# Performance work log

Measured on AMD Instinct MI355X. Metric: run time of the kernel, lower is better.

Reference implementation:

```python
import jax, jax.numpy as jnp
import numpy as np

N_NODES = 50000
N_EDGES = 800000
D = 128
NEG_SLOPE = 0.01
LN_EPS = 1e-5


def gcn_conv(x, W, b, src, dst, n_nodes):
    # Linear transform: [N, D_in] @ [D_in, D_out]
    h = x @ W
    # Symmetric degree normalization (self-loops already included in src/dst)
    deg = jax.ops.segment_sum(jnp.ones_like(dst, dtype=h.dtype), dst, num_segments=n_nodes)
    dinv = jnp.where(deg > 0, jax.lax.rsqrt(deg), 0.0)
    coef = dinv[src] * dinv[dst]                      # [E]
    msg = h[src] * coef[:, None]                      # gather + scale, [E, D]
    out = jax.ops.segment_sum(msg, dst, num_segments=n_nodes)  # scatter-add
    return out + b


def layer_norm(x, gamma, beta):
    mu = jnp.mean(x, axis=-1, keepdims=True)
    var = jnp.mean(jnp.square(x - mu), axis=-1, keepdims=True)
    return (x - mu) * jax.lax.rsqrt(var + LN_EPS) * gamma + beta


def setup_inputs() -> dict:
    key = jax.random.key(0)
    ks = jax.random.split(key, 8)
    x = jax.random.normal(ks[0], (N_NODES, D), dtype=jnp.float32)
    edge_index = jax.random.randint(ks[1], (2, N_EDGES), 0, N_NODES, dtype=jnp.int64)
    s = 1.0 / np.sqrt(D)
    W1 = jax.random.uniform(ks[2], (D, D), jnp.float32, -s, s)
    b1 = jnp.zeros((D,), jnp.float32)
    W2 = jax.random.uniform(ks[3], (D, D), jnp.float32, -s, s)
    b2 = jnp.zeros((D,), jnp.float32)
    ln1_g = jnp.ones((D,), jnp.float32)
    ln1_b = jnp.zeros((D,), jnp.float32)
    ln2_g = jnp.ones((D,), jnp.float32)
    ln2_b = jnp.zeros((D,), jnp.float32)
    return {"x": x, "edge_index": edge_index, "W1": W1, "b1": b1,
            "ln1_g": ln1_g, "ln1_b": ln1_b, "W2": W2, "b2": b2,
            "ln2_g": ln2_g, "ln2_b": ln2_b}


def reference(x, edge_index, W1, b1, ln1_g, ln1_b, W2, b2, ln2_g, ln2_b):
    n = x.shape[0]
    # add self-loops (PyG GCNConv default)
    loops = jnp.arange(n, dtype=edge_index.dtype)
    src = jnp.concatenate([edge_index[0], loops])
    dst = jnp.concatenate([edge_index[1], loops])

    residual = x
    h = gcn_conv(x, W1, b1, src, dst, n)
    h = jax.nn.leaky_relu(h, NEG_SLOPE)
    h = layer_norm(h + residual, ln1_g, ln1_b)
    h = gcn_conv(h, W2, b2, src, dst, n)
    return jax.nn.leaky_relu(layer_norm(h + residual, ln2_g, ln2_b), NEG_SLOPE)
```

## Files before the change

kernel.cpp:

```cpp
#include <hip/hip_runtime.h>
#include <hip/hip_bf16.h>

#define NN 50000
#define NE 800000
#define D 128
#define NEG_SLOPE 0.01f
#define LN_EPS 1e-5f

#define NPB 256
#define NB 196
#define CAP 6144
#define ECH 8192
#define NCH ((NE + ECH - 1) / ECH)

typedef __attribute__((ext_vector_type(8))) short bf16x8;
typedef __attribute__((ext_vector_type(4))) float f32x4;
typedef __attribute__((ext_vector_type(4))) int i32x4;

__device__ inline unsigned short f2bf(float f) {
    unsigned u = __float_as_uint(f);
    unsigned r = 0x7FFFu + ((u >> 16) & 1u);
    return (unsigned short)((u + r) >> 16);
}
__device__ inline void bf2x(unsigned u, float& lo, float& hi) {
    lo = __uint_as_float(u << 16);
    hi = __uint_as_float(u & 0xFFFF0000u);
}


__global__ __launch_bounds__(256) void bucket_scatter(const int* __restrict__ src,
                                                      const int* __restrict__ dst,
                                                      int* __restrict__ bcursor,
                                                      int2* __restrict__ bedge, int ne) {
    __shared__ int2 stage[ECH];
    __shared__ int hist[NB], lofs[NB], lcur[NB], gbase[NB];
    __shared__ int tmp[256];
    int t = threadIdx.x;
    int e0 = blockIdx.x * ECH;
    int ecnt = min(ECH, ne - e0);
    if (t < NB) hist[t] = 0;
    __syncthreads();
    for (int k = t; k < ecnt; k += 256) atomicAdd(&hist[dst[e0 + k] >> 8], 1);
    __syncthreads();
    int v = (t < NB) ? hist[t] : 0;
    tmp[t] = v;
    __syncthreads();
    for (int off = 1; off < 256; off <<= 1) {
        int u = (t >= off) ? tmp[t - off] : 0;
        __syncthreads();
        tmp[t] += u;
        __syncthreads();
    }
    if (t < NB) {
        lofs[t] = tmp[t] - v;
        lcur[t] = tmp[t] - v;
        gbase[t] = atomicAdd(&bcursor[t], v);
    }
    __syncthreads();
    for (int k = t; k < ecnt; k += 256) {
        int s = src[e0 + k], d = dst[e0 + k];
        int p = atomicAdd(&lcur[d >> 8], 1);
        stage[p] = make_int2(s, d);
    }
    __syncthreads();
    for (int k = t; k < ecnt; k += 256) {
        int2 eg = stage[k];
        int b = eg.y >> 8;
        bedge[(size_t)b * CAP + gbase[b] + (k - lofs[b])] = eg;
    }
}

__global__ __launch_bounds__(256) void node_count(const int2* __restrict__ bedge,
                                                  const int* __restrict__ bcnt,
                                                  float* __restrict__ dinv,
                                                  int2* __restrict__ rowinfo,
                                                  int* __restrict__ ticket) {
    __shared__ int h[NPB];
    __shared__ int tmp[256];
    __shared__ int base;
    int b = blockIdx.x, t = threadIdx.x;
    h[t] = 0;
    __syncthreads();
    int s0 = b * CAP, s1 = s0 + bcnt[b];
    for (int k = s0 + t; k < s1; k += 256) atomicAdd(&h[bedge[k].y & 255], 1);
    __syncthreads();
    int deg = h[t];
    int node = b * NPB + t;
    int pdeg = (deg + 7) & ~7;
    tmp[t] = pdeg;
    __syncthreads();
    for (int off = 1; off < 256; off <<= 1) {
        int u = (t >= off) ? tmp[t - off] : 0;
        __syncthreads();
        tmp[t] += u;
        __syncthreads();
    }
    if (t == 255) base = atomicAdd(ticket, tmp[255]);
    __syncthreads();
    if (node < NN) {
        dinv[node] = rsqrtf((float)(deg + 1));
        rowinfo[node] = make_int2(base + tmp[t] - pdeg, pdeg);
    }
}

__global__ __launch_bounds__(256) void csr_scatter(const int2* __restrict__ bedge,
                                                   const int* __restrict__ bcnt,
                                                   const int2* __restrict__ rowinfo,
                                                   const float* __restrict__ dinv,
                                                   int2* __restrict__ csr_pair) {
    __shared__ int cur[NPB];
    __shared__ int rl[NPB];
    int b = blockIdx.x, t = threadIdx.x;
    int node = b * NPB + t;
    rl[t] = (node < NN) ? rowinfo[node].x : 0;
    cur[t] = 0;
    __syncthreads();
    int s0 = b * CAP, s1 = s0 + bcnt[b];
    for (int k = s0 + t; k < s1; k += 256) {
        int2 eg = bedge[k];
        int li = eg.y & 255;
        int p = atomicAdd(&cur[li], 1);
        float coef = dinv[eg.x] * dinv[eg.y];
        csr_pair[rl[li] + p] = make_int2(eg.x, __float_as_int(coef));
    }
    __syncthreads();
    int deg = cur[t];
    int pend = (deg + 7) & ~7;
    int selfsrc = (node < NN) ? node : 0;
    for (int k = deg; k < pend; ++k)
        csr_pair[rl[t] + k] = make_int2(selfsrc, 0);
}

__global__ void wt_pack2(const float* __restrict__ W1, const float* __restrict__ W2,
                         unsigned short* __restrict__ WT1, unsigned short* __restrict__ WT2) {
    int tid = blockIdx.x * 256 + threadIdx.x;
    const float* W = (tid < D * D) ? W1 : W2;
    unsigned short* WT = (tid < D * D) ? WT1 : WT2;
    int id = tid & (D * D - 1);
    int nn = id & 127, k = id >> 7;
    WT[nn * 128 + k] = f2bf(W[k * 128 + nn]);
}

template <bool BF16IN>
__global__ __launch_bounds__(256) void gemm_mfma(const void* __restrict__ Ain,
                                                 const unsigned short* __restrict__ WT,
                                                 unsigned short* __restrict__ out, int n) {
    __shared__ __align__(16) unsigned short a_lds[64 * 128];
    __shared__ __align__(16) unsigned short w_lds[128 * 128];
    int t = threadIdx.x;
    int m0 = blockIdx.x * 64;

    #pragma unroll
    for (int it = 0; it < 8; ++it) {
        int idx = it * 256 + t;
        int row = idx >> 4, c = idx & 15;
        uint4 v = *(const uint4*)&WT[row * 128 + c * 8];
        int byte = (row * 256 + c * 16) ^ ((row & 7) << 4);
        *(uint4*)((char*)w_lds + byte) = v;
    }
    #pragma unroll
    for (int it = 0; it < 4; ++it) {
        int idx = it * 256 + t;
        int row = idx >> 4, c = idx & 15;
        int grow = m0 + row;
        uint4 w = make_uint4(0u, 0u, 0u, 0u);
        if (grow < n) {
            if constexpr (BF16IN) {
                w = *(const uint4*)&((const unsigned short*)Ain)[(size_t)grow * D + c * 8];
            } else {
                const float* Af = (const float*)Ain;
                float4 v0 = *(const float4*)&Af[(size_t)grow * D + c * 8];
                float4 v1 = *(const float4*)&Af[(size_t)grow * D + c * 8 + 4];
                w.x = (unsigned)f2bf(v0.x) | ((unsigned)f2bf(v0.y) << 16);
                w.y = (unsigned)f2bf(v0.z) | ((unsigned)f2bf(v0.w) << 16);
                w.z = (unsigned)f2bf(v1.x) | ((unsigned)f2bf(v1.y) << 16);
                w.w = (unsigned)f2bf(v1.z) | ((unsigned)f2bf(v1.w) << 16);
            }
        }
        int byte = (row * 256 + c * 16) ^ ((row & 7) << 4);
        *(uint4*)((char*)a_lds + byte) = w;
    }
    __syncthreads();

    int wv = t >> 6, l = t & 63;
    int lrow = l & 15, lgrp = l >> 4;
    int arow = wv * 16 + lrow;

    f32x4 acc[8];
    #pragma unroll
    for (int nf = 0; nf < 8; ++nf) acc[nf] = (f32x4){0.f, 0.f, 0.f, 0.f};

    #pragma unroll
    for (int kk = 0; kk < 4; ++kk) {
        int abyte = (arow * 256 + kk * 64 + lgrp * 16) ^ ((arow & 7) << 4);
        bf16x8 afrag = *(bf16x8*)((char*)a_lds + abyte);
        #pragma unroll
        for (int nf = 0; nf < 8; ++nf) {
            int bcol = nf * 16 + lrow;
            int bbyte = (bcol * 256 + kk * 64 + lgrp * 16) ^ ((bcol & 7) << 4);
            bf16x8 bfrag = *(bf16x8*)((char*)w_lds + bbyte);
            acc[nf] = __builtin_amdgcn_mfma_f32_16x16x32_bf16(afrag, bfrag, acc[nf], 0, 0, 0);
        }
    }

    #pragma unroll
    for (int nf = 0; nf < 8; ++nf) {
        #pragma unroll
        for (int r = 0; r < 4; ++r) {
            int grow = m0 + wv * 16 + lgrp * 4 + r;
            if (grow < n) {
                int col = nf * 16 + lrow;
                out[(size_t)grow * D + col] = f2bf(acc[nf][r]);
            }
        }
    }
}


__device__ inline void agg8(const unsigned* __restrict__ h, const int2* __restrict__ csr_pair,
                            int e, int lane, float& accx, float& accy) {
    i32x4 q0 = __builtin_nontemporal_load((const i32x4*)(csr_pair + e + 0));
    i32x4 q1 = __builtin_nontemporal_load((const i32x4*)(csr_pair + e + 2));
    i32x4 q2 = __builtin_nontemporal_load((const i32x4*)(csr_pair + e + 4));
    i32x4 q3 = __builtin_nontemporal_load((const i32x4*)(csr_pair + e + 6));
    unsigned g0 = h[(size_t)q0[0] * (D / 2) + lane];
    unsigned g1 = h[(size_t)q0[2] * (D / 2) + lane];
    unsigned g2 = h[(size_t)q1[0] * (D / 2) + lane];
    unsigned g3 = h[(size_t)q1[2] * (D / 2) + lane];
    unsigned g4 = h[(size_t)q2[0] * (D / 2) + lane];
    unsigned g5 = h[(size_t)q2[2] * (D / 2) + lane];
    unsigned g6 = h[(size_t)q3[0] * (D / 2) + lane];
    unsigned g7 = h[(size_t)q3[2] * (D / 2) + lane];
    float ax, ay, c;
    c = __int_as_float(q0[1]); bf2x(g0, ax, ay); accx = fmaf(c, ax, accx); accy = fmaf(c, ay, accy);
    c = __int_as_float(q0[3]); bf2x(g1, ax, ay); accx = fmaf(c, ax, accx); accy = fmaf(c, ay, accy);
    c = __int_as_float(q1[1]); bf2x(g2, ax, ay); accx = fmaf(c, ax, accx); accy = fmaf(c, ay, accy);
    c = __int_as_float(q1[3]); bf2x(g3, ax, ay); accx = fmaf(c, ax, accx); accy = fmaf(c, ay, accy);
    c = __int_as_float(q2[1]); bf2x(g4, ax, ay); accx = fmaf(c, ax, accx); accy = fmaf(c, ay, accy);
    c = __int_as_float(q2[3]); bf2x(g5, ax, ay); accx = fmaf(c, ax, accx); accy = fmaf(c, ay, accy);
    c = __int_as_float(q3[1]); bf2x(g6, ax, ay); accx = fmaf(c, ax, accx); accy = fmaf(c, ay, accy);
    c = __int_as_float(q3[3]); bf2x(g7, ax, ay); accx = fmaf(c, ax, accx); accy = fmaf(c, ay, accy);
}

template <int MODE>
__global__ __launch_bounds__(256) void agg_ln(const unsigned* __restrict__ h,
                                              const float* __restrict__ x,
                                              const float* __restrict__ bias,
                                              const float* __restrict__ gamma,
                                              const float* __restrict__ beta,
                                              const float* __restrict__ dinv,
                                              const int2* __restrict__ rowinfo,
                                              const int2* __restrict__ csr_pair,
                                              float* __restrict__ out,
                                              unsigned* __restrict__ outb) {
    int wid = threadIdx.x >> 6;
    int lane = threadIdx.x & 63;
    int iA = blockIdx.x * 8 + wid * 2;
    int iB = iA + 1;
    float diA = dinv[iA], diB = dinv[iB];

    float hx, hy;
    bf2x(h[(size_t)iA * (D / 2) + lane], hx, hy);
    float aAx = diA * diA * hx, aAy = diA * diA * hy;
    bf2x(h[(size_t)iB * (D / 2) + lane], hx, hy);
    float aBx = diB * diB * hx, aBy = diB * diB * hy;

    int2 riA = rowinfo[iA];
    int2 riB = rowinfo[iB];
    int eA = __builtin_amdgcn_readfirstlane(riA.x);
    int eA1 = eA + __builtin_amdgcn_readfirstlane(riA.y);
    int eB = __builtin_amdgcn_readfirstlane(riB.x);
    int eB1 = eB + __builtin_amdgcn_readfirstlane(riB.y);

    while (eA < eA1 && eB < eB1) {
        i32x4 qA0 = __builtin_nontemporal_load((const i32x4*)(csr_pair + eA + 0));
        i32x4 qA1 = __builtin_nontemporal_load((const i32x4*)(csr_pair + eA + 2));
        i32x4 qA2 = __builtin_nontemporal_load((const i32x4*)(csr_pair + eA + 4));
        i32x4 qA3 = __builtin_nontemporal_load((const i32x4*)(csr_pair + eA + 6));
        i32x4 qB0 = __builtin_nontemporal_load((const i32x4*)(csr_pair + eB + 0));
        i32x4 qB1 = __builtin_nontemporal_load((const i32x4*)(csr_pair + eB + 2));
        i32x4 qB2 = __builtin_nontemporal_load((const i32x4*)(csr_pair + eB + 4));
        i32x4 qB3 = __builtin_nontemporal_load((const i32x4*)(csr_pair + eB + 6));
        unsigned gA0 = h[(size_t)qA0[0] * (D / 2) + lane];
        unsigned gA1 = h[(size_t)qA0[2] * (D / 2) + lane];
        unsigned gA2 = h[(size_t)qA1[0] * (D / 2) + lane];
        unsigned gA3 = h[(size_t)qA1[2] * (D / 2) + lane];
        unsigned gA4 = h[(size_t)qA2[0] * (D / 2) + lane];
        unsigned gA5 = h[(size_t)qA2[2] * (D / 2) + lane];
        unsigned gA6 = h[(size_t)qA3[0] * (D / 2) + lane];
        unsigned gA7 = h[(size_t)qA3[2] * (D / 2) + lane];
        unsigned gB0 = h[(size_t)qB0[0] * (D / 2) + lane];
        unsigned gB1 = h[(size_t)qB0[2] * (D / 2) + lane];
        unsigned gB2 = h[(size_t)qB1[0] * (D / 2) + lane];
        unsigned gB3 = h[(size_t)qB1[2] * (D / 2) + lane];
        unsigned gB4 = h[(size_t)qB2[0] * (D / 2) + lane];
        unsigned gB5 = h[(size_t)qB2[2] * (D / 2) + lane];
        unsigned gB6 = h[(size_t)qB3[0] * (D / 2) + lane];
        unsigned gB7 = h[(size_t)qB3[2] * (D / 2) + lane];
        float ax, ay, c;
        c = __int_as_float(qA0[1]); bf2x(gA0, ax, ay); aAx = fmaf(c, ax, aAx); aAy = fmaf(c, ay, aAy);
        c = __int_as_float(qA0[3]); bf2x(gA1, ax, ay); aAx = fmaf(c, ax, aAx); aAy = fmaf(c, ay, aAy);
        c = __int_as_float(qA1[1]); bf2x(gA2, ax, ay); aAx = fmaf(c, ax, aAx); aAy = fmaf(c, ay, aAy);
        c = __int_as_float(qA1[3]); bf2x(gA3, ax, ay); aAx = fmaf(c, ax, aAx); aAy = fmaf(c, ay, aAy);
        c = __int_as_float(qA2[1]); bf2x(gA4, ax, ay); aAx = fmaf(c, ax, aAx); aAy = fmaf(c, ay, aAy);
        c = __int_as_float(qA2[3]); bf2x(gA5, ax, ay); aAx = fmaf(c, ax, aAx); aAy = fmaf(c, ay, aAy);
        c = __int_as_float(qA3[1]); bf2x(gA6, ax, ay); aAx = fmaf(c, ax, aAx); aAy = fmaf(c, ay, aAy);
        c = __int_as_float(qA3[3]); bf2x(gA7, ax, ay); aAx = fmaf(c, ax, aAx); aAy = fmaf(c, ay, aAy);
        c = __int_as_float(qB0[1]); bf2x(gB0, ax, ay); aBx = fmaf(c, ax, aBx); aBy = fmaf(c, ay, aBy);
        c = __int_as_float(qB0[3]); bf2x(gB1, ax, ay); aBx = fmaf(c, ax, aBx); aBy = fmaf(c, ay, aBy);
        c = __int_as_float(qB1[1]); bf2x(gB2, ax, ay); aBx = fmaf(c, ax, aBx); aBy = fmaf(c, ay, aBy);
        c = __int_as_float(qB1[3]); bf2x(gB3, ax, ay); aBx = fmaf(c, ax, aBx); aBy = fmaf(c, ay, aBy);
        c = __int_as_float(qB2[1]); bf2x(gB4, ax, ay); aBx = fmaf(c, ax, aBx); aBy = fmaf(c, ay, aBy);
        c = __int_as_float(qB2[3]); bf2x(gB5, ax, ay); aBx = fmaf(c, ax, aBx); aBy = fmaf(c, ay, aBy);
        c = __int_as_float(qB3[1]); bf2x(gB6, ax, ay); aBx = fmaf(c, ax, aBx); aBy = fmaf(c, ay, aBy);
        c = __int_as_float(qB3[3]); bf2x(gB7, ax, ay); aBx = fmaf(c, ax, aBx); aBy = fmaf(c, ay, aBy);
        eA += 8; eB += 8;
    }
    while (eA < eA1) { agg8(h, csr_pair, eA, lane, aAx, aAy); eA += 8; }
    while (eB < eB1) { agg8(h, csr_pair, eB, lane, aBx, aBy); eB += 8; }

    float2 bv = *(const float2*)&bias[2 * lane];
    float2 gv = *(const float2*)&gamma[2 * lane];
    float2 bt = *(const float2*)&beta[2 * lane];

    aAx += bv.x; aAy += bv.y;
    aBx += bv.x; aBy += bv.y;
    if (MODE == 0) {
        aAx = aAx > 0.f ? aAx : NEG_SLOPE * aAx;
        aAy = aAy > 0.f ? aAy : NEG_SLOPE * aAy;
        aBx = aBx > 0.f ? aBx : NEG_SLOPE * aBx;
        aBy = aBy > 0.f ? aBy : NEG_SLOPE * aBy;
    }
    size_t rowA = (size_t)iA * D + 2 * lane;
    size_t rowB = (size_t)iB * D + 2 * lane;
    float2 xA = *(const float2*)&x[rowA];
    float2 xB = *(const float2*)&x[rowB];
    float vA0 = aAx + xA.x, vA1 = aAy + xA.y;
    float vB0 = aBx + xB.x, vB1 = aBy + xB.y;

    float sA1 = vA0 + vA1, sA2 = vA0 * vA0 + vA1 * vA1;
    float sB1 = vB0 + vB1, sB2 = vB0 * vB0 + vB1 * vB1;
    #pragma unroll
    for (int off = 1; off < 64; off <<= 1) {
        sA1 += __shfl_xor(sA1, off, 64);
        sA2 += __shfl_xor(sA2, off, 64);
        sB1 += __shfl_xor(sB1, off, 64);
        sB2 += __shfl_xor(sB2, off, 64);
    }
    float muA = sA1 * (1.f / 128.f);
    float varA = fmaxf(sA2 * (1.f / 128.f) - muA * muA, 0.f);
    float rsA = rsqrtf(varA + LN_EPS);
    float muB = sB1 * (1.f / 128.f);
    float varB = fmaxf(sB2 * (1.f / 128.f) - muB * muB, 0.f);
    float rsB = rsqrtf(varB + LN_EPS);

    float oA0 = (vA0 - muA) * rsA * gv.x + bt.x;
    float oA1 = (vA1 - muA) * rsA * gv.y + bt.y;
    float oB0 = (vB0 - muB) * rsB * gv.x + bt.x;
    float oB1 = (vB1 - muB) * rsB * gv.y + bt.y;

    if (MODE == 0) {
        outb[(size_t)iA * (D / 2) + lane] = (unsigned)f2bf(oA0) | ((unsigned)f2bf(oA1) << 16);
        outb[(size_t)iB * (D / 2) + lane] = (unsigned)f2bf(oB0) | ((unsigned)f2bf(oB1) << 16);
    } else {
        oA0 = oA0 > 0.f ? oA0 : NEG_SLOPE * oA0;
        oA1 = oA1 > 0.f ? oA1 : NEG_SLOPE * oA1;
        oB0 = oB0 > 0.f ? oB0 : NEG_SLOPE * oB0;
        oB1 = oB1 > 0.f ? oB1 : NEG_SLOPE * oB1;
        *(float2*)&out[rowA] = make_float2(oA0, oA1);
        *(float2*)&out[rowB] = make_float2(oB0, oB1);
    }
}

extern "C" void kernel_launch(void* const* d_in, const int* in_sizes, int n_in,
                              void* d_out, int out_size, void* d_ws, size_t ws_size,
                              hipStream_t stream) {
    const float* x    = (const float*)d_in[0];
    const int*   ei   = (const int*)d_in[1];
    const float* W1   = (const float*)d_in[2];
    const float* b1   = (const float*)d_in[3];
    const float* ln1g = (const float*)d_in[4];
    const float* ln1b = (const float*)d_in[5];
    const float* W2   = (const float*)d_in[6];
    const float* b2   = (const float*)d_in[7];
    const float* ln2g = (const float*)d_in[8];
    const float* ln2b = (const float*)d_in[9];
    float* out = (float*)d_out;

    const int* srcp = ei;
    const int* dstp = ei + NE;

    char* ws = (char*)d_ws;
    size_t p = 0;
    auto alloc = [&](size_t bytes) {
        char* r = ws + p;
        p += (bytes + 255) & ~(size_t)255;
        return r;
    };
    int*   bcursor  = (int*)alloc((NB + 1) * 4);
    int2*  rowinfo  = (int2*)alloc((size_t)NN * 8);
    float* dinv     = (float*)alloc(NN * 4);
    int2*  bedge    = (int2*)alloc((size_t)NB * CAP * 8);
    int2*  csr_pair = (int2*)alloc(((size_t)NE + 8 * NN) * 8);
    unsigned short* hbf  = (unsigned short*)alloc((size_t)NN * D * 2);
    unsigned*       t1bf = (unsigned*)alloc((size_t)NN * D * 2);
    unsigned short* wt1  = (unsigned short*)alloc(D * D * 2);
    unsigned short* wt2  = (unsigned short*)alloc(D * D * 2);

    hipMemsetAsync(bcursor, 0, (NB + 1) * 4, stream);

    bucket_scatter<<<NCH, 256, 0, stream>>>(srcp, dstp, bcursor, bedge, NE);
    node_count<<<NB, 256, 0, stream>>>(bedge, bcursor, dinv, rowinfo, &bcursor[NB]);
    csr_scatter<<<NB, 256, 0, stream>>>(bedge, bcursor, rowinfo, dinv, csr_pair);

    wt_pack2<<<2 * D * D / 256, 256, 0, stream>>>(W1, W2, wt1, wt2);

    gemm_mfma<false><<<(NN + 63) / 64, 256, 0, stream>>>(x, wt1, hbf, NN);
    agg_ln<0><<<NN / 8, 256, 0, stream>>>((const unsigned*)hbf, x, b1, ln1g, ln1b, dinv,
                                          rowinfo, csr_pair, out, t1bf);

    gemm_mfma<true><<<(NN + 63) / 64, 256, 0, stream>>>(t1bf, wt2, hbf, NN);
    agg_ln<1><<<NN / 8, 256, 0, stream>>>((const unsigned*)hbf, x, b2, ln2g, ln2b, dinv,
                                          rowinfo, csr_pair, out, t1bf);
}
```

Measured before the change: 148.1 us.

## Fuse graph build with first GEMM and second GEMM into layer-1 aggregation

Edge bucketing, a global-atomic degree count and the first GEMM now run as independent block ranges inside one launch. Node counting and CSR scatter are merged into one kernel that reads degrees directly. The second GEMM is fused into the layer-1 aggregation/LayerNorm kernel, using 512-thread blocks that stage 16 normalized rows in LDS and run MFMA against W2 held in LDS. This cuts the launch count and removes the round trip of the intermediate bf16 activation through global memory. The cost is global atomics on degrees and reloading the 32KB W2 tile in every 16-row block.

```diff
diff --git a/kernel.cpp b/kernel.cpp
--- a/kernel.cpp
+++ b/kernel.cpp
@@ -10,8 +10,10 @@
 #define NPB 256
 #define NB 196
 #define CAP 6144
-#define ECH 8192
+#define ECH 6144
 #define NCH ((NE + ECH - 1) / ECH)
+#define NDEG 256
+#define NGEMM ((NN + 63) / 64)
 
 typedef __attribute__((ext_vector_type(8))) short bf16x8;
 typedef __attribute__((ext_vector_type(4))) float f32x4;
@@ -28,106 +30,180 @@
 }
 
 
-__global__ __launch_bounds__(256) void bucket_scatter(const int* __restrict__ src,
-                                                      const int* __restrict__ dst,
-                                                      int* __restrict__ bcursor,
-                                                      int2* __restrict__ bedge, int ne) {
-    __shared__ int2 stage[ECH];
-    __shared__ int hist[NB], lofs[NB], lcur[NB], gbase[NB];
+struct BucketLDS {
+    int2 stage[ECH];
+    int hist[NB], lofs[NB], lcur[NB], gbase[NB];
+    int tmp[256];
+};
+struct GemmLDS {
+    unsigned short a[64 * 128];
+    unsigned short w[128 * 128];
+};
+union FusedLDS { BucketLDS b; GemmLDS g; };
+
+__device__ inline void gemm_body(GemmLDS& L, const float* __restrict__ A,
+                                 const unsigned short* __restrict__ WT,
+                                 unsigned short* __restrict__ out, int m0, int n, int t) {
+    #pragma unroll
+    for (int it = 0; it < 8; ++it) {
+        int idx = it * 256 + t;
+        int row = idx >> 4, c = idx & 15;
+        uint4 v = *(const uint4*)&WT[row * 128 + c * 8];
+        int byte = (row * 256 + c * 16) ^ ((row & 7) << 4);
+        *(uint4*)((char*)L.w + byte) = v;
+    }
+    #pragma unroll
+    for (int it = 0; it < 4; ++it) {
+        int idx = it * 256 + t;
+        int row = idx >> 4, c = idx & 15;
+        int grow = m0 + row;
+        uint4 w = make_uint4(0u, 0u, 0u, 0u);
+        if (grow < n) {
+            float4 v0 = *(const float4*)&A[(size_t)grow * D + c * 8];
+            float4 v1 = *(const float4*)&A[(size_t)grow * D + c * 8 + 4];
+            w.x = (unsigned)f2bf(v0.x) | ((unsigned)f2bf(v0.y) << 16);
+            w.y = (unsigned)f2bf(v0.z) | ((unsigned)f2bf(v0.w) << 16);
+            w.z = (unsigned)f2bf(v1.x) | ((unsigned)f2bf(v1.y) << 16);
+            w.w = (unsigned)f2bf(v1.z) | ((unsigned)f2bf(v1.w) << 16);
+        }
+        int byte = (row * 256 + c * 16) ^ ((row & 7) << 4);
+        *(uint4*)((char*)L.a + byte) = w;
+    }
+    __syncthreads();
+
+    int wv = t >> 6, l = t & 63;
+    int lrow = l & 15, lgrp = l >> 4;
+    int arow = wv * 16 + lrow;
+
+    f32x4 acc[8];
+    #pragma unroll
+    for (int nf = 0; nf < 8; ++nf) acc[nf] = (f32x4){0.f, 0.f, 0.f, 0.f};
+
+    #pragma unroll
+    for (int kk = 0; kk < 4; ++kk) {
+        int abyte = (arow * 256 + kk * 64 + lgrp * 16) ^ ((arow & 7) << 4);
+        bf16x8 afrag = *(bf16x8*)((char*)L.a + abyte);
+        #pragma unroll
+        for (int nf = 0; nf < 8; ++nf) {
+            int bcol = nf * 16 + lrow;
+            int bbyte = (bcol * 256 + kk * 64 + lgrp * 16) ^ ((bcol & 7) << 4);
+            bf16x8 bfrag = *(bf16x8*)((char*)L.w + bbyte);
+            acc[nf] = __builtin_amdgcn_mfma_f32_16x16x32_bf16(afrag, bfrag, acc[nf], 0, 0, 0);
+        }
+    }
+
+    #pragma unroll
+    for (int nf = 0; nf < 8; ++nf) {
+        #pragma unroll
+        for (int r = 0; r < 4; ++r) {
+            int grow = m0 + wv * 16 + lgrp * 4 + r;
+            if (grow < n) out[(size_t)grow * D + nf * 16 + lrow] = f2bf(acc[nf][r]);
+        }
+    }
+}
+
+__global__ __launch_bounds__(256) void fused1(const int* __restrict__ src,
+                                              const int* __restrict__ dst,
+                                              int* __restrict__ bcursor,
+                                              int2* __restrict__ bedge,
+                                              int* __restrict__ deg,
+                                              const float* __restrict__ x,
+                                              const unsigned short* __restrict__ wt1,
+                                              unsigned short* __restrict__ hbf) {
+    __shared__ FusedLDS u;
+    int bid = blockIdx.x, t = threadIdx.x;
+
+    if (bid < NCH) {
+        BucketLDS& L = u.b;
+        int e0 = bid * ECH;
+        int ecnt = min(ECH, NE - e0);
+        if (t < NB) L.hist[t] = 0;
+        __syncthreads();
+        for (int k = t; k < ecnt; k += 256) atomicAdd(&L.hist[dst[e0 + k] >> 8], 1);
+        __syncthreads();
+        int v = (t < NB) ? L.hist[t] : 0;
+        L.tmp[t] = v;
+        __syncthreads();
+        for (int off = 1; off < 256; off <<= 1) {
+            int uu = (t >= off) ? L.tmp[t - off] : 0;
+            __syncthreads();
+            L.tmp[t] += uu;
+            __syncthreads();
+        }
+        if (t < NB) {
+            L.lofs[t] = L.tmp[t] - v;
+            L.lcur[t] = L.tmp[t] - v;
+            L.gbase[t] = atomicAdd(&bcursor[t], v);
+        }
+        __syncthreads();
+        for (int k = t; k < ecnt; k += 256) {
+            int s = src[e0 + k], d = dst[e0 + k];
+            int p = atomicAdd(&L.lcur[d >> 8], 1);
+            L.stage[p] = make_int2(s, d);
+        }
+        __syncthreads();
+        for (int k = t; k < ecnt; k += 256) {
+            int2 eg = L.stage[k];
+            int b = eg.y >> 8;
+            bedge[(size_t)b * CAP + L.gbase[b] + (k - L.lofs[b])] = eg;
+        }
+    } else if (bid < NCH + NDEG) {
+        for (int k = (bid - NCH) * 256 + t; k < NE; k += NDEG * 256)
+            atomicAdd(&deg[dst[k]], 1);
+    } else {
+        gemm_body(u.g, x, wt1, hbf, (bid - NCH - NDEG) * 64, NN, t);
+    }
+}
+
+__global__ __launch_bounds__(256) void fused2(const int2* __restrict__ bedge,
+                                              const int* __restrict__ bcnt,
+                                              const int* __restrict__ deg,
+                                              float* __restrict__ dinv,
+                                              int2* __restrict__ rowinfo,
+                                              int* __restrict__ ticket,
+                                              int2* __restrict__ csr_pair) {
     __shared__ int tmp[256];
-    int t = threadIdx.x;
-    int e0 = blockIdx.x * ECH;
-    int ecnt = min(ECH, ne - e0);
-    if (t < NB) hist[t] = 0;
-    __syncthreads();
-    for (int k = t; k < ecnt; k += 256) atomicAdd(&hist[dst[e0 + k] >> 8], 1);
-    __syncthreads();
-    int v = (t < NB) ? hist[t] : 0;
-    tmp[t] = v;
-    __syncthreads();
-    for (int off = 1; off < 256; off <<= 1) {
-        int u = (t >= off) ? tmp[t - off] : 0;
-        __syncthreads();
-        tmp[t] += u;
-        __syncthreads();
-    }
-    if (t < NB) {
-        lofs[t] = tmp[t] - v;
-        lcur[t] = tmp[t] - v;
-        gbase[t] = atomicAdd(&bcursor[t], v);
-    }
-    __syncthreads();
-    for (int k = t; k < ecnt; k += 256) {
-        int s = src[e0 + k], d = dst[e0 + k];
-        int p = atomicAdd(&lcur[d >> 8], 1);
-        stage[p] = make_int2(s, d);
-    }
-    __syncthreads();
-    for (int k = t; k < ecnt; k += 256) {
-        int2 eg = stage[k];
-        int b = eg.y >> 8;
-        bedge[(size_t)b * CAP + gbase[b] + (k - lofs[b])] = eg;
-    }
-}
-
-__global__ __launch_bounds__(256) void node_count(const int2* __restrict__ bedge,
-                                                  const int* __restrict__ bcnt,
-                                                  float* __restrict__ dinv,
-                                                  int2* __restrict__ rowinfo,
-                                                  int* __restrict__ ticket) {
-    __shared__ int h[NPB];
-    __shared__ int tmp[256];
+    __shared__ int rl[NPB], cur[NPB];
+    __shared__ float sdinv[NPB];
     __shared__ int base;
     int b = blockIdx.x, t = threadIdx.x;
-    h[t] = 0;
-    __syncthreads();
-    int s0 = b * CAP, s1 = s0 + bcnt[b];
-    for (int k = s0 + t; k < s1; k += 256) atomicAdd(&h[bedge[k].y & 255], 1);
-    __syncthreads();
-    int deg = h[t];
     int node = b * NPB + t;
-    int pdeg = (deg + 7) & ~7;
+    int dg = (node < NN) ? deg[node] : 0;
+    float dv = rsqrtf((float)(dg + 1));
+    sdinv[t] = dv;
+    int pdeg = (dg + 7) & ~7;
     tmp[t] = pdeg;
     __syncthreads();
     for (int off = 1; off < 256; off <<= 1) {
-        int u = (t >= off) ? tmp[t - off] : 0;
-        __syncthreads();
-        tmp[t] += u;
+        int uu = (t >= off) ? tmp[t - off] : 0;
+        __syncthreads();
+        tmp[t] += uu;
         __syncthreads();
     }
     if (t == 255) base = atomicAdd(ticket, tmp[255]);
     __syncthreads();
+    int start = base + tmp[t] - pdeg;
+    rl[t] = start;
+    cur[t] = 0;
     if (node < NN) {
-        dinv[node] = rsqrtf((float)(deg + 1));
-        rowinfo[node] = make_int2(base + tmp[t] - pdeg, pdeg);
-    }
-}
-
-__global__ __launch_bounds__(256) void csr_scatter(const int2* __restrict__ bedge,
-                                                   const int* __restrict__ bcnt,
-                                                   const int2* __restrict__ rowinfo,
-                                                   const float* __restrict__ dinv,
-                                                   int2* __restrict__ csr_pair) {
-    __shared__ int cur[NPB];
-    __shared__ int rl[NPB];
-    int b = blockIdx.x, t = threadIdx.x;
-    int node = b * NPB + t;
-    rl[t] = (node < NN) ? rowinfo[node].x : 0;
-    cur[t] = 0;
+        dinv[node] = dv;
+        rowinfo[node] = make_int2(start, pdeg);
+    }
     __syncthreads();
     int s0 = b * CAP, s1 = s0 + bcnt[b];
     for (int k = s0 + t; k < s1; k += 256) {
         int2 eg = bedge[k];
         int li = eg.y & 255;
         int p = atomicAdd(&cur[li], 1);
-        float coef = dinv[eg.x] * dinv[eg.y];
+        int ds = deg[eg.x];
+        float coef = rsqrtf((float)(ds + 1)) * sdinv[li];
         csr_pair[rl[li] + p] = make_int2(eg.x, __float_as_int(coef));
     }
     __syncthreads();
-    int deg = cur[t];
-    int pend = (deg + 7) & ~7;
+    int dgc = cur[t];
+    int pend = (dgc + 7) & ~7;
     int selfsrc = (node < NN) ? node : 0;
-    for (int k = deg; k < pend; ++k)
+    for (int k = dgc; k < pend; ++k)
         csr_pair[rl[t] + k] = make_int2(selfsrc, 0);
 }
 
@@ -139,81 +215,6 @@
     int id = tid & (D * D - 1);
     int nn = id & 127, k = id >> 7;
     WT[nn * 128 + k] = f2bf(W[k * 128 + nn]);
-}
-
-template <bool BF16IN>
-__global__ __launch_bounds__(256) void gemm_mfma(const void* __restrict__ Ain,
-                                                 const unsigned short* __restrict__ WT,
-                                                 unsigned short* __restrict__ out, int n) {
-    __shared__ __align__(16) unsigned short a_lds[64 * 128];
-    __shared__ __align__(16) unsigned short w_lds[128 * 128];
-    int t = threadIdx.x;
-    int m0 = blockIdx.x * 64;
-
-    #pragma unroll
-    for (int it = 0; it < 8; ++it) {
-        int idx = it * 256 + t;
-        int row = idx >> 4, c = idx & 15;
-        uint4 v = *(const uint4*)&WT[row * 128 + c * 8];
-        int byte = (row * 256 + c * 16) ^ ((row & 7) << 4);
-        *(uint4*)((char*)w_lds + byte) = v;
-    }
-    #pragma unroll
-    for (int it = 0; it < 4; ++it) {
-        int idx = it * 256 + t;
-        int row = idx >> 4, c = idx & 15;
-        int grow = m0 + row;
-        uint4 w = make_uint4(0u, 0u, 0u, 0u);
-        if (grow < n) {
-            if constexpr (BF16IN) {
-                w = *(const uint4*)&((const unsigned short*)Ain)[(size_t)grow * D + c * 8];
-            } else {
-                const float* Af = (const float*)Ain;
-                float4 v0 = *(const float4*)&Af[(size_t)grow * D + c * 8];
-                float4 v1 = *(const float4*)&Af[(size_t)grow * D + c * 8 + 4];
-                w.x = (unsigned)f2bf(v0.x) | ((unsigned)f2bf(v0.y) << 16);
-                w.y = (unsigned)f2bf(v0.z) | ((unsigned)f2bf(v0.w) << 16);
-                w.z = (unsigned)f2bf(v1.x) | ((unsigned)f2bf(v1.y) << 16);
-                w.w = (unsigned)f2bf(v1.z) | ((unsigned)f2bf(v1.w) << 16);
-            }
-        }
-        int byte = (row * 256 + c * 16) ^ ((row & 7) << 4);
-        *(uint4*)((char*)a_lds + byte) = w;
-    }
-    __syncthreads();
-
-    int wv = t >> 6, l = t & 63;
-    int lrow = l & 15, lgrp = l >> 4;
-    int arow = wv * 16 + lrow;
-
-    f32x4 acc[8];
-    #pragma unroll
-    for (int nf = 0; nf < 8; ++nf) acc[nf] = (f32x4){0.f, 0.f, 0.f, 0.f};
-
-    #pragma unroll
-    for (int kk = 0; kk < 4; ++kk) {
-        int abyte = (arow * 256 + kk * 64 + lgrp * 16) ^ ((arow & 7) << 4);
-        bf16x8 afrag = *(bf16x8*)((char*)a_lds + abyte);
-        #pragma unroll
-        for (int nf = 0; nf < 8; ++nf) {
-            int bcol = nf * 16 + lrow;
-            int bbyte = (bcol * 256 + kk * 64 + lgrp * 16) ^ ((bcol & 7) << 4);
-            bf16x8 bfrag = *(bf16x8*)((char*)w_lds + bbyte);
-            acc[nf] = __builtin_amdgcn_mfma_f32_16x16x32_bf16(afrag, bfrag, acc[nf], 0, 0, 0);
-        }
-    }
-
-    #pragma unroll
-    for (int nf = 0; nf < 8; ++nf) {
-        #pragma unroll
-        for (int r = 0; r < 4; ++r) {
-            int grow = m0 + wv * 16 + lgrp * 4 + r;
-            if (grow < n) {
-                int col = nf * 16 + lrow;
-                out[(size_t)grow * D + col] = f2bf(acc[nf][r]);
-            }
-        }
-    }
 }
 
 
@@ -242,36 +243,10 @@
     c = __int_as_float(q3[3]); bf2x(g7, ax, ay); accx = fmaf(c, ax, accx); accy = fmaf(c, ay, accy);
 }
 
-template <int MODE>
-__global__ __launch_bounds__(256) void agg_ln(const unsigned* __restrict__ h,
-                                              const float* __restrict__ x,
-                                              const float* __restrict__ bias,
-                                              const float* __restrict__ gamma,
-                                              const float* __restrict__ beta,
-                                              const float* __restrict__ dinv,
-                                              const int2* __restrict__ rowinfo,
-                                              const int2* __restrict__ csr_pair,
-                                              float* __restrict__ out,
-                                              unsigned* __restrict__ outb) {
-    int wid = threadIdx.x >> 6;
-    int lane = threadIdx.x & 63;
-    int iA = blockIdx.x * 8 + wid * 2;
-    int iB = iA + 1;
-    float diA = dinv[iA], diB = dinv[iB];
-
-    float hx, hy;
-    bf2x(h[(size_t)iA * (D / 2) + lane], hx, hy);
-    float aAx = diA * diA * hx, aAy = diA * diA * hy;
-    bf2x(h[(size_t)iB * (D / 2) + lane], hx, hy);
-    float aBx = diB * diB * hx, aBy = diB * diB * hy;
-
-    int2 riA = rowinfo[iA];
-    int2 riB = rowinfo[iB];
-    int eA = __builtin_amdgcn_readfirstlane(riA.x);
-    int eA1 = eA + __builtin_amdgcn_readfirstlane(riA.y);
-    int eB = __builtin_amdgcn_readfirstlane(riB.x);
-    int eB1 = eB + __builtin_amdgcn_readfirstlane(riB.y);
-
+__device__ inline void agg_2node(const unsigned* __restrict__ h,
+                                 const int2* __restrict__ csr_pair,
+                                 int eA, int eA1, int eB, int eB1, int lane,
+                                 float& aAx, float& aAy, float& aBx, float& aBy) {
     while (eA < eA1 && eB < eB1) {
         i32x4 qA0 = __builtin_nontemporal_load((const i32x4*)(csr_pair + eA + 0));
         i32x4 qA1 = __builtin_nontemporal_load((const i32x4*)(csr_pair + eA + 2));
@@ -318,6 +293,49 @@
     }
     while (eA < eA1) { agg8(h, csr_pair, eA, lane, aAx, aAy); eA += 8; }
     while (eB < eB1) { agg8(h, csr_pair, eB, lane, aBx, aBy); eB += 8; }
+}
+
+__global__ __launch_bounds__(512) void agg_ln1_gemm(const unsigned* __restrict__ h,
+                                                    const float* __restrict__ x,
+                                                    const float* __restrict__ bias,
+                                                    const float* __restrict__ gamma,
+                                                    const float* __restrict__ beta,
+                                                    const float* __restrict__ dinv,
+                                                    const int2* __restrict__ rowinfo,
+                                                    const int2* __restrict__ csr_pair,
+                                                    const unsigned short* __restrict__ wt2,
+                                                    unsigned short* __restrict__ hbf2) {
+    __shared__ __align__(16) unsigned short w_lds[128 * 128];
+    __shared__ __align__(16) unsigned short a_lds[16 * 128];
+    int t = threadIdx.x;
+
+    #pragma unroll
+    for (int it = 0; it < 4; ++it) {
+        int idx = it * 512 + t;
+        int row = idx >> 4, c = idx & 15;
+        uint4 v = *(const uint4*)&wt2[row * 128 + c * 8];
+        int byte = (row * 256 + c * 16) ^ ((row & 7) << 4);
+        *(uint4*)((char*)w_lds + byte) = v;
+    }
+
+    int wid = t >> 6, lane = t & 63;
+    int iA = blockIdx.x * 16 + wid * 2;
+    int iB = iA + 1;
+    float diA = dinv[iA], diB = dinv[iB];
+
+    float hx, hy;
+    bf2x(h[(size_t)iA * (D / 2) + lane], hx, hy);
+    float aAx = diA * diA * hx, aAy = diA * diA * hy;
+    bf2x(h[(size_t)iB * (D / 2) + lane], hx, hy);
+    float aBx = diB * diB * hx, aBy = diB * diB * hy;
+
+    int2 riA = rowinfo[iA];
+    int2 riB = rowinfo[iB];
+    int eA = __builtin_amdgcn_readfirstlane(riA.x);
+    int eA1 = eA + __builtin_amdgcn_readfirstlane(riA.y);
+    int eB = __builtin_amdgcn_readfirstlane(riB.x);
+    int eB1 = eB + __builtin_amdgcn_readfirstlane(riB.y);
+    agg_2node(h, csr_pair, eA, eA1, eB, eB1, lane, aAx, aAy, aBx, aBy);
 
     float2 bv = *(const float2*)&bias[2 * lane];
     float2 gv = *(const float2*)&gamma[2 * lane];
@@ -325,12 +343,11 @@
 
     aAx += bv.x; aAy += bv.y;
     aBx += bv.x; aBy += bv.y;
-    if (MODE == 0) {
-        aAx = aAx > 0.f ? aAx : NEG_SLOPE * aAx;
-        aAy = aAy > 0.f ? aAy : NEG_SLOPE * aAy;
-        aBx = aBx > 0.f ? aBx : NEG_SLOPE * aBx;
-        aBy = aBy > 0.f ? aBy : NEG_SLOPE * aBy;
-    }
+    aAx = aAx > 0.f ? aAx : NEG_SLOPE * aAx;
+    aAy = aAy > 0.f ? aAy : NEG_SLOPE * aAy;
+    aBx = aBx > 0.f ? aBx : NEG_SLOPE * aBx;
+    aBy = aBy > 0.f ? aBy : NEG_SLOPE * aBy;
+
     size_t rowA = (size_t)iA * D + 2 * lane;
     size_t rowB = (size_t)iB * D + 2 * lane;
     float2 xA = *(const float2*)&x[rowA];
@@ -359,17 +376,101 @@
     float oB0 = (vB0 - muB) * rsB * gv.x + bt.x;
     float oB1 = (vB1 - muB) * rsB * gv.y + bt.y;
 
-    if (MODE == 0) {
-        outb[(size_t)iA * (D / 2) + lane] = (unsigned)f2bf(oA0) | ((unsigned)f2bf(oA1) << 16);
-        outb[(size_t)iB * (D / 2) + lane] = (unsigned)f2bf(oB0) | ((unsigned)f2bf(oB1) << 16);
-    } else {
-        oA0 = oA0 > 0.f ? oA0 : NEG_SLOPE * oA0;
-        oA1 = oA1 > 0.f ? oA1 : NEG_SLOPE * oA1;
-        oB0 = oB0 > 0.f ? oB0 : NEG_SLOPE * oB0;
-        oB1 = oB1 > 0.f ? oB1 : NEG_SLOPE * oB1;
-        *(float2*)&out[rowA] = make_float2(oA0, oA1);
-        *(float2*)&out[rowB] = make_float2(oB0, oB1);
-    }
+    int rA = wid * 2, rB = wid * 2 + 1;
+    unsigned dwA = (unsigned)f2bf(oA0) | ((unsigned)f2bf(oA1) << 16);
+    unsigned dwB = (unsigned)f2bf(oB0) | ((unsigned)f2bf(oB1) << 16);
+    int byteA = (rA * 256 + lane * 4) ^ ((rA & 7) << 4);
+    int byteB = (rB * 256 + lane * 4) ^ ((rB & 7) << 4);
+    *(unsigned*)((char*)a_lds + byteA) = dwA;
+    *(unsigned*)((char*)a_lds + byteB) = dwB;
+    __syncthreads();
+
+    int lrow = lane & 15, lgrp = lane >> 4;
+    f32x4 acc = (f32x4){0.f, 0.f, 0.f, 0.f};
+    #pragma unroll
+    for (int kk = 0; kk < 4; ++kk) {
+        int abyte = (lrow * 256 + kk * 64 + lgrp * 16) ^ ((lrow & 7) << 4);
+        bf16x8 afrag = *(bf16x8*)((char*)a_lds + abyte);
+        int bcol = wid * 16 + lrow;
+        int bbyte = (bcol * 256 + kk * 64 + lgrp * 16) ^ ((bcol & 7) << 4);
+        bf16x8 bfrag = *(bf16x8*)((char*)w_lds + bbyte);
+        acc = __builtin_amdgcn_mfma_f32_16x16x32_bf16(afrag, bfrag, acc, 0, 0, 0);
+    }
+    #pragma unroll
+    for (int r = 0; r < 4; ++r) {
+        int grow = blockIdx.x * 16 + lgrp * 4 + r;
+        hbf2[(size_t)grow * D + wid * 16 + lrow] = f2bf(acc[r]);
+    }
+}
+
+__global__ __launch_bounds__(256) void agg_ln2(const unsigned* __restrict__ h,
+                                               const float* __restrict__ x,
+                                               const float* __restrict__ bias,
+                                               const float* __restrict__ gamma,
+                                               const float* __restrict__ beta,
+                                               const float* __restrict__ dinv,
+                                               const int2* __restrict__ rowinfo,
+                                               const int2* __restrict__ csr_pair,
+                                               float* __restrict__ out) {
+    int wid = threadIdx.x >> 6;
+    int lane = threadIdx.x & 63;
+    int iA = blockIdx.x * 8 + wid * 2;
+    int iB = iA + 1;
+    float diA = dinv[iA], diB = dinv[iB];
+
+    float hx, hy;
+    bf2x(h[(size_t)iA * (D / 2) + lane], hx, hy);
+    float aAx = diA * diA * hx, aAy = diA * diA * hy;
+    bf2x(h[(size_t)iB * (D / 2) + lane], hx, hy);
+    float aBx = diB * diB * hx, aBy = diB * diB * hy;
+
+    int2 riA = rowinfo[iA];
+    int2 riB = rowinfo[iB];
+    int eA = __builtin_amdgcn_readfirstlane(riA.x);
+    int eA1 = eA + __builtin_amdgcn_readfirstlane(riA.y);
+    int eB = __builtin_amdgcn_readfirstlane(riB.x);
+    int eB1 = eB + __builtin_amdgcn_readfirstlane(riB.y);
+    agg_2node(h, csr_pair, eA, eA1, eB, eB1, lane, aAx, aAy, aBx, aBy);
+
+    float2 bv = *(const float2*)&bias[2 * lane];
+    float2 gv = *(const float2*)&gamma[2 * lane];
+    float2 bt = *(const float2*)&beta[2 * lane];
+
+    aAx += bv.x; aAy += bv.y;
+    aBx += bv.x; aBy += bv.y;
+    size_t rowA = (size_t)iA * D + 2 * lane;
+    size_t rowB = (size_t)iB * D + 2 * lane;
+    float2 xA = *(const float2*)&x[rowA];
+    float2 xB = *(const float2*)&x[rowB];
+    float vA0 = aAx + xA.x, vA1 = aAy + xA.y;
+    float vB0 = aBx + xB.x, vB1 = aBy + xB.y;
+
+    float sA1 = vA0 + vA1, sA2 = vA0 * vA0 + vA1 * vA1;
+    float sB1 = vB0 + vB1, sB2 = vB0 * vB0 + vB1 * vB1;
+    #pragma unroll
+    for (int off = 1; off < 64; off <<= 1) {
+        sA1 += __shfl_xor(sA1, off, 64);
+        sA2 += __shfl_xor(sA2, off, 64);
+        sB1 += __shfl_xor(sB1, off, 64);
+        sB2 += __shfl_xor(sB2, off, 64);
+    }
+    float muA = sA1 * (1.f / 128.f);
+    float varA = fmaxf(sA2 * (1.f / 128.f) - muA * muA, 0.f);
+    float rsA = rsqrtf(varA + LN_EPS);
+    float muB = sB1 * (1.f / 128.f);
+    float varB = fmaxf(sB2 * (1.f / 128.f) - muB * muB, 0.f);
+    float rsB = rsqrtf(varB + LN_EPS);
+
+    float oA0 = (vA0 - muA) * rsA * gv.x + bt.x;
+    float oA1 = (vA1 - muA) * rsA * gv.y + bt.y;
+    float oB0 = (vB0 - muB) * rsB * gv.x + bt.x;
+    float oB1 = (vB1 - muB) * rsB * gv.y + bt.y;
+    oA0 = oA0 > 0.f ? oA0 : NEG_SLOPE * oA0;
+    oA1 = oA1 > 0.f ? oA1 : NEG_SLOPE * oA1;
+    oB0 = oB0 > 0.f ? oB0 : NEG_SLOPE * oB0;
+    oB1 = oB1 > 0.f ? oB1 : NEG_SLOPE * oB1;
+    *(float2*)&out[rowA] = make_float2(oA0, oA1);
+    *(float2*)&out[rowB] = make_float2(oB0, oB1);
 }
 
 extern "C" void kernel_launch(void* const* d_in, const int* in_sizes, int n_in,
@@ -397,29 +498,31 @@
         p += (bytes + 255) & ~(size_t)255;
         return r;
     };
+    int*   deg      = (int*)alloc(NN * 4);
     int*   bcursor  = (int*)alloc((NB + 1) * 4);
     int2*  rowinfo  = (int2*)alloc((size_t)NN * 8);
     float* dinv     = (float*)alloc(NN * 4);
     int2*  bedge    = (int2*)alloc((size_t)NB * CAP * 8);
     int2*  csr_pair = (int2*)alloc(((size_t)NE + 8 * NN) * 8);
     unsigned short* hbf  = (unsigned short*)alloc((size_t)NN * D * 2);
-    unsigned*       t1bf = (unsigned*)alloc((size_t)NN * D * 2);
+    unsigned short* hbf2 = (unsigned short*)alloc((size_t)NN * D * 2);
     unsigned short* wt1  = (unsigned short*)alloc(D * D * 2);
     unsigned short* wt2  = (unsigned short*)alloc(D * D * 2);
 
-    hipMemsetAsync(bcursor, 0, (NB + 1) * 4, stream);
-
-    bucket_scatter<<<NCH, 256, 0, stream>>>(srcp, dstp, bcursor, bedge, NE);
-    node_count<<<NB, 256, 0, stream>>>(bedge, bcursor, dinv, rowinfo, &bcursor[NB]);
-    csr_scatter<<<NB, 256, 0, stream>>>(bedge, bcursor, rowinfo, dinv, csr_pair);
+    size_t zbytes = (char*)rowinfo - (char*)deg;
+    hipMemsetAsync(deg, 0, zbytes, stream);
 
     wt_pack2<<<2 * D * D / 256, 256, 0, stream>>>(W1, W2, wt1, wt2);
 
-    gemm_mfma<false><<<(NN + 63) / 64, 256, 0, stream>>>(x, wt1, hbf, NN);
-    agg_ln<0><<<NN / 8, 256, 0, stream>>>((const unsigned*)hbf, x, b1, ln1g, ln1b, dinv,
-                                          rowinfo, csr_pair, out, t1bf);
-
-    gemm_mfma<true><<<(NN + 63) / 64, 256, 0, stream>>>(t1bf, wt2, hbf, NN);
-    agg_ln<1><<<NN / 8, 256, 0, stream>>>((const unsigned*)hbf, x, b2, ln2g, ln2b, dinv,
-                                          rowinfo, csr_pair, out, t1bf);
-}
+    fused1<<<NCH + NDEG + NGEMM, 256, 0, stream>>>(srcp, dstp, bcursor, bedge, deg,
+                                                   x, wt1, hbf);
+
+    fused2<<<NB, 256, 0, stream>>>(bedge, bcursor, deg, dinv, rowinfo,
+                                   &bcursor[NB], csr_pair);
+
+    agg_ln1_gemm<<<NN / 16, 512, 0, stream>>>((const unsigned*)hbf, x, b1, ln1g, ln1b,
+                                              dinv, rowinfo, csr_pair, wt2, hbf2);
+
+    agg_ln2<<<NN / 8, 256, 0, stream>>>((const unsigned*)hbf2, x, b2, ln2g, ln2b,
+                                        dinv, rowinfo, csr_pair, out);
+}
```

Result: faster. 143.4 us (-3.2%).
